# Kernel tuning notes

Measured on AMD Instinct MI355X. Metric: run time of the kernel, lower is better.

Reference implementation:

```python
import jax, jax.numpy as jnp
import numpy as np

B, S, D, H = 8, 1024, 768, 12
DH = D // H
EPS = 1e-5


def setup_inputs() -> dict:
    key = jax.random.key(0)
    ks = jax.random.split(key, 12)
    sc_h = 1.0 / np.sqrt(DH)
    sc_d = 1.0 / np.sqrt(D)
    return {
        "x": jax.random.normal(ks[0], (B, S, D), jnp.float32),
        "ln1_g": jnp.ones((D,), jnp.float32),
        "ln1_b": jnp.zeros((D,), jnp.float32),
        "Wq": jax.random.normal(ks[1], (H, DH, DH), jnp.float32) * sc_h,
        "bq": jax.random.normal(ks[2], (H, DH), jnp.float32) * 0.01,
        "Wk": jax.random.normal(ks[3], (H, DH, DH), jnp.float32) * sc_h,
        "bk": jax.random.normal(ks[4], (H, DH), jnp.float32) * 0.01,
        "Wv": jax.random.normal(ks[5], (H, DH, DH), jnp.float32) * sc_h,
        "bv": jax.random.normal(ks[6], (H, DH), jnp.float32) * 0.01,
        "ln2_g": jnp.ones((D,), jnp.float32),
        "ln2_b": jnp.zeros((D,), jnp.float32),
        "W1": jax.random.normal(ks[7], (D, 4 * D), jnp.float32) * sc_d,  # c_fc (bias=False)
        "W2": jax.random.normal(ks[8], (4 * D, D), jnp.float32) * (1.0 / np.sqrt(4 * D)),  # c_proj (bias=False)
    }


def _layernorm(x, g, b):
    m = jnp.mean(x, axis=-1, keepdims=True)
    v = jnp.mean(jnp.square(x - m), axis=-1, keepdims=True)
    return (x - m) * jax.lax.rsqrt(v + EPS) * g + b


def _msa(x, Wq, bq, Wk, bk, Wv, bv):
    b, s, d = x.shape
    h = x.reshape(b, s, H, DH)  # per-head slices of the embedding
    q = jnp.einsum('bshd,hde->bhse', h, Wq) + bq[None, :, None, :]
    k = jnp.einsum('bshd,hde->bhse', h, Wk) + bk[None, :, None, :]
    v = jnp.einsum('bshd,hde->bhse', h, Wv) + bv[None, :, None, :]
    scores = jnp.einsum('bhse,bhte->bhst', q, k) / np.sqrt(DH).astype(np.float32)
    attn = jax.nn.softmax(scores, axis=-1)
    o = jnp.einsum('bhst,bhte->bhse', attn, v)
    return o.transpose(0, 2, 1, 3).reshape(b, s, d)  # concat heads


def reference(x, ln1_g, ln1_b, Wq, bq, Wk, bk, Wv, bv, ln2_g, ln2_b, W1, W2):
    out = x + _msa(_layernorm(x, ln1_g, ln1_b), Wq, bq, Wk, bk, Wv, bv)
    h = _layernorm(out, ln2_g, ln2_b)
    ffn = jnp.dot(jax.nn.gelu(jnp.dot(h, W1), approximate=False), W2)
    return out + ffn
```

## Files before the change

kernel.cpp:

```cpp
#include <hip/hip_runtime.h>
#include <hip/hip_bf16.h>
#include <math.h>

#define B_ 8
#define S_ 1024
#define D_ 768
#define H_ 12
#define QSCALE 0.18033688011112042f

typedef __attribute__((ext_vector_type(8))) short short8;
typedef __attribute__((ext_vector_type(4))) float floatx4;
typedef unsigned short ushort_t;

__device__ __forceinline__ ushort_t f2bf(float f) {
  unsigned int u = __builtin_bit_cast(unsigned int, f);
  u += 0x7fffu + ((u >> 16) & 1u);
  return (ushort_t)(u >> 16);
}

__device__ __forceinline__ unsigned int pkbf(float a, float b) {
  __hip_bfloat162 h = __float22bfloat162_rn(make_float2(a, b));
  unsigned int r;
  __builtin_memcpy(&r, &h, sizeof(r));
  return r;
}

__global__ __launch_bounds__(256) void ln_bf16(
    const float* __restrict__ in, const float* __restrict__ g,
    const float* __restrict__ bias, ushort_t* __restrict__ out) {
  const int row = blockIdx.x * 4 + (threadIdx.x >> 6);
  const int lane = threadIdx.x & 63;
  const float* p = in + (size_t)row * D_;
  float4 v[3];
#pragma unroll
  for (int j = 0; j < 3; ++j) v[j] = *(const float4*)(p + j * 256 + lane * 4);
  float s = 0.f;
#pragma unroll
  for (int j = 0; j < 3; ++j) s += (v[j].x + v[j].y) + (v[j].z + v[j].w);
#pragma unroll
  for (int m = 1; m < 64; m <<= 1) s += __shfl_xor(s, m);
  const float mean = s * (1.0f / D_);
  float q = 0.f;
#pragma unroll
  for (int j = 0; j < 3; ++j) {
    const float a = v[j].x - mean, b = v[j].y - mean;
    const float c = v[j].z - mean, d = v[j].w - mean;
    q += (a * a + b * b) + (c * c + d * d);
  }
#pragma unroll
  for (int m = 1; m < 64; m <<= 1) q += __shfl_xor(q, m);
  const float rstd = rsqrtf(q * (1.0f / D_) + 1e-5f);
  ushort_t* o = out + (size_t)row * D_;
#pragma unroll
  for (int j = 0; j < 3; ++j) {
    const float4 gv = *(const float4*)(g + j * 256 + lane * 4);
    const float4 bv = *(const float4*)(bias + j * 256 + lane * 4);
    const unsigned int p01 = pkbf((v[j].x - mean) * rstd * gv.x + bv.x,
                                  (v[j].y - mean) * rstd * gv.y + bv.y);
    const unsigned int p23 = pkbf((v[j].z - mean) * rstd * gv.z + bv.z,
                                  (v[j].w - mean) * rstd * gv.w + bv.w);
    *(uint2*)(o + j * 256 + lane * 4) = make_uint2(p01, p23);
  }
}

__global__ __launch_bounds__(256) void transpose_cast(
    const float* __restrict__ W, ushort_t* __restrict__ Wt, int Kdim, int Ndim) {
  __shared__ float tile[32][33];
  const int n0 = blockIdx.x * 32, k0 = blockIdx.y * 32;
  const int tx = threadIdx.x & 31, ty = threadIdx.x >> 5;
#pragma unroll
  for (int i = 0; i < 32; i += 8)
    tile[ty + i][tx] = W[(size_t)(k0 + ty + i) * Ndim + n0 + tx];
  __syncthreads();
#pragma unroll
  for (int i = 0; i < 32; i += 8)
    Wt[(size_t)(n0 + ty + i) * Kdim + k0 + tx] = f2bf(tile[tx][ty + i]);
}

__global__ __launch_bounds__(256) void trans_w64(
    const float* __restrict__ Wq, const float* __restrict__ Wk,
    const float* __restrict__ Wv, ushort_t* __restrict__ Wqt,
    ushort_t* __restrict__ Wkt, ushort_t* __restrict__ Wvt) {
  const int h = blockIdx.x;
  const float* W = blockIdx.y == 0 ? Wq : blockIdx.y == 1 ? Wk : Wv;
  ushort_t* O = blockIdx.y == 0 ? Wqt : blockIdx.y == 1 ? Wkt : Wvt;
  __shared__ float t[64][65];
  const int tid = threadIdx.x;
#pragma unroll
  for (int i = 0; i < 16; ++i) {
    const int idx = tid + i * 256;
    t[idx >> 6][idx & 63] = W[h * 4096 + idx];
  }
  __syncthreads();
#pragma unroll
  for (int i = 0; i < 16; ++i) {
    const int idx = tid + i * 256;
    O[h * 4096 + idx] = f2bf(t[idx & 63][idx >> 6]);
  }
}

__global__ __launch_bounds__(256) void qkv_mfma(
    const ushort_t* __restrict__ xbf,
    const ushort_t* __restrict__ Wqt, const ushort_t* __restrict__ Wkt,
    const ushort_t* __restrict__ Wvt,
    const float* __restrict__ bq, const float* __restrict__ bk,
    const float* __restrict__ bv,
    ushort_t* __restrict__ qo, ushort_t* __restrict__ ko,
    ushort_t* __restrict__ vt) {
  const int h = blockIdx.y;
  const int mb = blockIdx.x * 128;
  const int tid = threadIdx.x;
  const int wave = tid >> 6, lane = tid & 63;
  const int lc = lane & 15, kq = lane >> 4;
  const int wm = wave * 32;

  short8 af[2][2];
#pragma unroll
  for (int mi = 0; mi < 2; ++mi)
#pragma unroll
    for (int kc = 0; kc < 2; ++kc)
      af[mi][kc] = *(const short8*)(xbf + (size_t)(mb + wm + mi * 16 + lc) * D_ +
                                    h * 64 + kc * 32 + kq * 8);

  const ushort_t* Wp[3] = {Wqt + h * 4096, Wkt + h * 4096, Wvt + h * 4096};
  floatx4 acc[3][2][4] = {};
#pragma unroll
  for (int w3 = 0; w3 < 3; ++w3)
#pragma unroll
    for (int n = 0; n < 4; ++n)
#pragma unroll
      for (int kc = 0; kc < 2; ++kc) {
        const short8 bfv =
            *(const short8*)(Wp[w3] + (n * 16 + lc) * 64 + kc * 32 + kq * 8);
#pragma unroll
        for (int mi = 0; mi < 2; ++mi)
          acc[w3][mi][n] = __builtin_amdgcn_mfma_f32_16x16x32_bf16(
              af[mi][kc], bfv, acc[w3][mi][n], 0, 0, 0);
      }

  const int b = mb >> 10;
  const size_t obase = (size_t)(b * H_ + h) * (S_ * 64);
#pragma unroll
  for (int w3 = 0; w3 < 2; ++w3) {
    const float* bias = (w3 == 0 ? bq : bk) + h * 64;
    ushort_t* outp = w3 == 0 ? qo : ko;
#pragma unroll
    for (int n = 0; n < 4; ++n) {
      const int e = n * 16 + lc;
      const float bvv = bias[e];
#pragma unroll
      for (int mi = 0; mi < 2; ++mi)
#pragma unroll
        for (int r = 0; r < 4; ++r) {
          const int sl = (mb & 1023) + wm + mi * 16 + kq * 4 + r;
          float v = acc[w3][mi][n][r] + bvv;
          if (w3 == 0) v *= QSCALE;
          outp[obase + (size_t)sl * 64 + e] = f2bf(v);
        }
    }
  }
#pragma unroll
  for (int n = 0; n < 4; ++n) {
    const int e = n * 16 + lc;
    const float bvv = bv[h * 64 + e];
#pragma unroll
    for (int mi = 0; mi < 2; ++mi) {
      const int sl0 = (mb & 1023) + wm + mi * 16 + kq * 4;
      const unsigned int p01 =
          pkbf(acc[2][mi][n][0] + bvv, acc[2][mi][n][1] + bvv);
      const unsigned int p23 =
          pkbf(acc[2][mi][n][2] + bvv, acc[2][mi][n][3] + bvv);
      *(uint2*)(vt + obase + (size_t)e * S_ + sl0) = make_uint2(p01, p23);
    }
  }
}

__global__ __launch_bounds__(256) void attn_mfma(
    const ushort_t* __restrict__ qb, const ushort_t* __restrict__ kb,
    const ushort_t* __restrict__ vt, const float* __restrict__ x,
    float* __restrict__ out1) {
  const int bh = blockIdx.x;
  const int tid = threadIdx.x;
  const int wave = tid >> 6, lane = tid & 63;
  const int lc = lane & 15, kq = lane >> 4;
  const int q0 = blockIdx.y * 128 + wave * 32;

  __shared__ __align__(16) ushort_t Ks[64 * 64];
  __shared__ __align__(16) ushort_t Vs[64 * 64];
  __shared__ __align__(16) ushort_t Pw[4][2][16 * 72];

  const ushort_t* qp = qb + (size_t)bh * (S_ * 64);
  const ushort_t* kp = kb + (size_t)bh * (S_ * 64);
  const ushort_t* vp = vt + (size_t)bh * (S_ * 64);

  short8 qf[2][2];
#pragma unroll
  for (int qi = 0; qi < 2; ++qi)
#pragma unroll
    for (int kc = 0; kc < 2; ++kc)
      qf[qi][kc] = *(const short8*)(qp + (size_t)(q0 + qi * 16 + lc) * 64 +
                                    kc * 32 + kq * 8);

  const int srow = tid >> 3;
  const int sgc = ((tid & 7) ^ (srow & 7)) * 8;
  const int slds = srow * 64 + (tid & 7) * 8;
  const int swz = lc & 7;

  float l_r[2] = {0.0f, 0.0f};
  floatx4 oacc[2][4] = {};

  for (int kt = 0; kt < 16; ++kt) {
#pragma unroll
    for (int half = 0; half < 2; ++half) {
      const int r = half * 32 + srow;
      __builtin_amdgcn_global_load_lds(
          (const __attribute__((address_space(1))) unsigned int*)
              (kp + (size_t)(kt * 64 + r) * 64 + sgc),
          (__attribute__((address_space(3))) unsigned int*)
              (Ks + half * 2048 + slds), 16, 0, 0);
      __builtin_amdgcn_global_load_lds(
          (const __attribute__((address_space(1))) unsigned int*)
              (vp + (size_t)r * S_ + kt * 64 + sgc),
          (__attribute__((address_space(3))) unsigned int*)
              (Vs + half * 2048 + slds), 16, 0, 0);
    }
    __syncthreads();

    floatx4 sacc[2][4] = {};
#pragma unroll
    for (int mi = 0; mi < 4; ++mi) {
      const int row = (mi * 16 + lc) * 64;
#pragma unroll
      for (int kc = 0; kc < 2; ++kc) {
        const short8 kf =
            *(const short8*)(Ks + row + ((kc * 4 + kq) ^ swz) * 8);
        sacc[0][mi] = __builtin_amdgcn_mfma_f32_16x16x32_bf16(
            kf, qf[0][kc], sacc[0][mi], 0, 0, 0);
        sacc[1][mi] = __builtin_amdgcn_mfma_f32_16x16x32_bf16(
            kf, qf[1][kc], sacc[1][mi], 0, 0, 0);
      }
    }

#pragma unroll
    for (int qi = 0; qi < 2; ++qi) {
      float pr[4][4];
      float sm = 0.f;
#pragma unroll
      for (int mi = 0; mi < 4; ++mi)
#pragma unroll
        for (int r = 0; r < 4; ++r) {
          pr[mi][r] = exp2f(sacc[qi][mi][r]);
          sm += pr[mi][r];
        }
      l_r[qi] += sm;
#pragma unroll
      for (int mi = 0; mi < 4; ++mi) {
        const unsigned int p01 = pkbf(pr[mi][0], pr[mi][1]);
        const unsigned int p23 = pkbf(pr[mi][2], pr[mi][3]);
        *(uint2*)(&Pw[wave][qi][lc * 72 + mi * 16 + kq * 4]) =
            make_uint2(p01, p23);
      }
    }
    asm volatile("s_waitcnt lgkmcnt(0)" ::: "memory");

    short8 pf[2][2];
#pragma unroll
    for (int qi = 0; qi < 2; ++qi)
#pragma unroll
      for (int kc = 0; kc < 2; ++kc)
        pf[qi][kc] =
            *(const short8*)(&Pw[wave][qi][lc * 72 + kc * 32 + kq * 8]);
#pragma unroll
    for (int mi = 0; mi < 4; ++mi) {
      const int row = (mi * 16 + lc) * 64;
#pragma unroll
      for (int kc = 0; kc < 2; ++kc) {
        const short8 vf =
            *(const short8*)(Vs + row + ((kc * 4 + kq) ^ swz) * 8);
        oacc[0][mi] = __builtin_amdgcn_mfma_f32_16x16x32_bf16(
            vf, pf[0][kc], oacc[0][mi], 0, 0, 0);
        oacc[1][mi] = __builtin_amdgcn_mfma_f32_16x16x32_bf16(
            vf, pf[1][kc], oacc[1][mi], 0, 0, 0);
      }
    }
    __syncthreads();
  }

  const int b = bh / H_, h = bh % H_;
  float* Ow = (float*)&Pw[wave][0][0];
#pragma unroll
  for (int qi = 0; qi < 2; ++qi) {
    float lt = l_r[qi];
    lt += __shfl_xor(lt, 16);
    lt += __shfl_xor(lt, 32);
    const float inv = 1.0f / lt;
#pragma unroll
    for (int mi = 0; mi < 4; ++mi) {
      floatx4 ov = oacc[qi][mi];
      ov[0] *= inv; ov[1] *= inv; ov[2] *= inv; ov[3] *= inv;
      *(floatx4*)(&Ow[lc * 68 + mi * 16 + kq * 4]) = ov;
    }
    asm volatile("s_waitcnt lgkmcnt(0)" ::: "memory");
    const int row = (lane >> 3) & 7, c8 = (lane & 7) * 4;
#pragma unroll
    for (int rg = 0; rg < 2; ++rg) {
      const int qq = rg * 8 + row;
      const size_t gbase =
          ((size_t)(b * S_) + q0 + qi * 16 + qq) * D_ + h * 64 + c8;
#pragma unroll
      for (int j = 0; j < 2; ++j) {
        const float4 ov = *(const float4*)(&Ow[qq * 68 + j * 32 + c8]);
        const float4 xv = *(const float4*)(x + gbase + j * 32);
        *(float4*)(out1 + gbase + j * 32) =
            make_float4(ov.x + xv.x, ov.y + xv.y, ov.z + xv.z, ov.w + xv.w);
      }
    }
    asm volatile("s_waitcnt lgkmcnt(0)" ::: "memory");
  }
}

template <int N, int K, bool GELU, bool RESID, bool OUT_BF16>
__global__ __launch_bounds__(256) void mfma_gemm(
    const ushort_t* __restrict__ A, const ushort_t* __restrict__ Bt,
    const float* __restrict__ resid, void* __restrict__ Cout) {
  const int mb = blockIdx.y * 128;
  const int nb = blockIdx.x * 128;
  const int tid = threadIdx.x;
  const int wave = tid >> 6, lane = tid & 63;
  const int wm = (wave >> 1) * 64, wn = (wave & 1) * 64;

  __shared__ ushort_t Asp[128 * 32];
  __shared__ ushort_t Bsp[128 * 32];

  const int srow = wave * 16 + (lane >> 2);
  const int skoff = (lane & 3) * 8;

  floatx4 acc[4][4] = {};

  for (int kb = 0; kb < K; kb += 32) {
#pragma unroll
    for (int j = 0; j < 2; ++j) {
      const int row = j * 64 + srow;
      __builtin_amdgcn_global_load_lds(
          (const __attribute__((address_space(1))) unsigned int*)
              (A + (size_t)(mb + row) * K + kb + skoff),
          (__attribute__((address_space(3))) unsigned int*)
              (Asp + (size_t)row * 32 + skoff),
          16, 0, 0);
      __builtin_amdgcn_global_load_lds(
          (const __attribute__((address_space(1))) unsigned int*)
              (Bt + (size_t)(nb + row) * K + kb + skoff),
          (__attribute__((address_space(3))) unsigned int*)
              (Bsp + (size_t)row * 32 + skoff),
          16, 0, 0);
    }
    __syncthreads();

    const short8* As8 = (const short8*)Asp;
    const short8* Bs8 = (const short8*)Bsp;
    const int lrow = lane & 15, lkq = lane >> 4;
    short8 af[4], bfr[4];
#pragma unroll
    for (int i = 0; i < 4; ++i) {
      af[i]  = As8[(wm + i * 16 + lrow) * 4 + lkq];
      bfr[i] = Bs8[(wn + i * 16 + lrow) * 4 + lkq];
    }
#pragma unroll
    for (int i = 0; i < 4; ++i)
#pragma unroll
      for (int j = 0; j < 4; ++j)
        acc[i][j] = __builtin_amdgcn_mfma_f32_16x16x32_bf16(
            af[i], bfr[j], acc[i][j], 0, 0, 0);
    __syncthreads();
  }

  const int lcol = lane & 15, lr4 = (lane >> 4) * 4;
#pragma unroll
  for (int i = 0; i < 4; ++i)
#pragma unroll
    for (int r = 0; r < 4; ++r) {
      const int m = mb + wm + i * 16 + lr4 + r;
#pragma unroll
      for (int j = 0; j < 4; ++j) {
        const int col = nb + wn + j * 16 + lcol;
        float vv = acc[i][j][r];
        if (GELU) vv = 0.5f * vv * (1.0f + erff(vv * 0.70710678f));
        if (RESID) vv += resid[(size_t)m * N + col];
        if (OUT_BF16)
          ((ushort_t*)Cout)[(size_t)m * N + col] = f2bf(vv);
        else
          ((float*)Cout)[(size_t)m * N + col] = vv;
      }
    }
}

template <int N, int K>
__global__ __launch_bounds__(256) void mfma_gemm2(
    const ushort_t* __restrict__ A, const ushort_t* __restrict__ Bt,
    const float* __restrict__ resid, float* __restrict__ C) {
  const int lin = blockIdx.x;
  const int xcd = lin & 7, slot = lin >> 3;
  const int mbg = slot / 6, nbi = slot - mbg * 6;
  const int mb = (xcd * 16 + mbg) * 64;
  const int nb = nbi * 128;
  const int tid = threadIdx.x;
  const int wave = tid >> 6, lane = tid & 63;
  const int wm = (wave >> 1) * 32, wn = (wave & 1) * 64;

  __shared__ __align__(16) ushort_t Asp[64 * 64];
  __shared__ __align__(16) ushort_t Bsp[128 * 64];

  const int sr = tid >> 3;
  const int sc8 = (tid & 7) * 8;
  const int sgx = ((tid & 7) ^ (sr & 7)) * 8;

  floatx4 acc[2][4] = {};

  for (int kb = 0; kb < K; kb += 64) {
#pragma unroll
    for (int j = 0; j < 2; ++j) {
      const int row = j * 32 + sr;
      __builtin_amdgcn_global_load_lds(
          (const __attribute__((address_space(1))) unsigned int*)
              (A + (size_t)(mb + row) * K + kb + sgx),
          (__attribute__((address_space(3))) unsigned int*)
              (Asp + row * 64 + sc8), 16, 0, 0);
    }
#pragma unroll
    for (int j = 0; j < 4; ++j) {
      const int row = j * 32 + sr;
      __builtin_amdgcn_global_load_lds(
          (const __attribute__((address_space(1))) unsigned int*)
              (Bt + (size_t)(nb + row) * K + kb + sgx),
          (__attribute__((address_space(3))) unsigned int*)
              (Bsp + row * 64 + sc8), 16, 0, 0);
    }
    __syncthreads();

    const int lc = lane & 15, kq = lane >> 4, swz = lc & 7;
    short8 af[2][2], bfr[4][2];
#pragma unroll
    for (int i = 0; i < 2; ++i)
#pragma unroll
      for (int ks = 0; ks < 2; ++ks)
        af[i][ks] = *(const short8*)(Asp + (wm + i * 16 + lc) * 64 +
                                     ((ks * 4 + kq) ^ swz) * 8);
#pragma unroll
    for (int j = 0; j < 4; ++j)
#pragma unroll
      for (int ks = 0; ks < 2; ++ks)
        bfr[j][ks] = *(const short8*)(Bsp + (wn + j * 16 + lc) * 64 +
                                      ((ks * 4 + kq) ^ swz) * 8);
#pragma unroll
    for (int ks = 0; ks < 2; ++ks)
#pragma unroll
      for (int i = 0; i < 2; ++i)
#pragma unroll
        for (int j = 0; j < 4; ++j)
          acc[i][j] = __builtin_amdgcn_mfma_f32_16x16x32_bf16(
              af[i][ks], bfr[j][ks], acc[i][j], 0, 0, 0);
    __syncthreads();
  }

  const int lcol = lane & 15, lr4 = (lane >> 4) * 4;
#pragma unroll
  for (int i = 0; i < 2; ++i)
#pragma unroll
    for (int r = 0; r < 4; ++r) {
      const int m = mb + wm + i * 16 + lr4 + r;
#pragma unroll
      for (int j = 0; j < 4; ++j) {
        const int col = nb + wn + j * 16 + lcol;
        C[(size_t)m * N + col] =
            acc[i][j][r] + resid[(size_t)m * N + col];
      }
    }
}

extern "C" void kernel_launch(void* const* d_in, const int* in_sizes, int n_in,
                              void* d_out, int out_size, void* d_ws, size_t ws_size,
                              hipStream_t stream) {
  (void)in_sizes; (void)n_in; (void)out_size; (void)ws_size;
  const float* x     = (const float*)d_in[0];
  const float* ln1_g = (const float*)d_in[1];
  const float* ln1_b = (const float*)d_in[2];
  const float* Wq    = (const float*)d_in[3];
  const float* bq    = (const float*)d_in[4];
  const float* Wk    = (const float*)d_in[5];
  const float* bk    = (const float*)d_in[6];
  const float* Wv    = (const float*)d_in[7];
  const float* bv    = (const float*)d_in[8];
  const float* ln2_g = (const float*)d_in[9];
  const float* ln2_b = (const float*)d_in[10];
  const float* W1    = (const float*)d_in[11];
  const float* W2    = (const float*)d_in[12];
  float* out = (float*)d_out;

  const size_t n = (size_t)B_ * S_ * D_;
  ushort_t* u = (ushort_t*)d_ws;
  ushort_t* xbf  = u;
  ushort_t* qb   = xbf + n;
  ushort_t* kb   = qb + n;
  ushort_t* vt   = kb + n;
  ushort_t* xbf2 = vt + n;
  ushort_t* act  = xbf2 + n;
  ushort_t* Wt1  = act + (size_t)8192 * 3072;
  ushort_t* Wt2  = Wt1 + (size_t)3072 * 768;
  ushort_t* Wqt  = Wt2 + (size_t)768 * 3072;
  ushort_t* Wkt  = Wqt + H_ * 4096;
  ushort_t* Wvt  = Wkt + H_ * 4096;
  float* out1 = (float*)(Wvt + H_ * 4096);

  trans_w64<<<dim3(12, 3), dim3(256), 0, stream>>>(Wq, Wk, Wv, Wqt, Wkt, Wvt);
  transpose_cast<<<dim3(96, 24), dim3(256), 0, stream>>>(W1, Wt1, 768, 3072);
  transpose_cast<<<dim3(24, 96), dim3(256), 0, stream>>>(W2, Wt2, 3072, 768);
  ln_bf16<<<dim3(2048), dim3(256), 0, stream>>>(x, ln1_g, ln1_b, xbf);
  qkv_mfma<<<dim3(64, 12), dim3(256), 0, stream>>>(xbf, Wqt, Wkt, Wvt,
                                                   bq, bk, bv, qb, kb, vt);
  attn_mfma<<<dim3(96, 8), dim3(256), 0, stream>>>(qb, kb, vt, x, out1);
  ln_bf16<<<dim3(2048), dim3(256), 0, stream>>>(out1, ln2_g, ln2_b, xbf2);
  mfma_gemm<3072, 768, true, false, true>
      <<<dim3(24, 64), dim3(256), 0, stream>>>(xbf2, Wt1, nullptr, act);
  mfma_gemm2<768, 3072>
      <<<dim3(768), dim3(256), 0, stream>>>(act, Wt2, out1, out);
}
```

Baseline: 306.2 us.

## Unify FFN GEMMs into double-buffered pipelined kernel with fast GELU

```diff
diff --git a/kernel.cpp b/kernel.cpp
--- a/kernel.cpp
+++ b/kernel.cpp
@@ -23,6 +23,28 @@
   unsigned int r;
   __builtin_memcpy(&r, &h, sizeof(r));
   return r;
+}
+
+__device__ __forceinline__ float gelu_f(float x) {
+  const float z = fabsf(x) * 0.70710678118654752f;
+  const float t = __builtin_amdgcn_rcpf(1.0f + 0.3275911f * z);
+  const float p =
+      t * (0.254829592f +
+           t * (-0.284496736f +
+                t * (1.421413741f + t * (-1.453152027f + t * 1.061405429f))));
+  const float e = __expf(-z * z);
+  const float erfv = 1.0f - p * e;
+  return 0.5f * x * (1.0f + copysignf(erfv, x));
+}
+
+template <int N>
+__device__ __forceinline__ void wait_vmcnt() {
+  if constexpr (N == 0)
+    asm volatile("s_waitcnt vmcnt(0)" ::: "memory");
+  else if constexpr (N == 6)
+    asm volatile("s_waitcnt vmcnt(6)" ::: "memory");
+  else
+    asm volatile("s_waitcnt vmcnt(8)" ::: "memory");
 }
 
 __global__ __launch_bounds__(256) void ln_bf16(
@@ -319,160 +341,128 @@
   }
 }
 
-template <int N, int K, bool GELU, bool RESID, bool OUT_BF16>
-__global__ __launch_bounds__(256) void mfma_gemm(
+template <int BM, int BN, int N, int K, bool GELU, bool RESID, bool OUT_BF16,
+          bool XCDMAP>
+__global__ __launch_bounds__(256) void gemm_pipe(
     const ushort_t* __restrict__ A, const ushort_t* __restrict__ Bt,
     const float* __restrict__ resid, void* __restrict__ Cout) {
-  const int mb = blockIdx.y * 128;
-  const int nb = blockIdx.x * 128;
+  constexpr int MI = BM / 32;
+  constexpr int NJ = BN / 32;
+  constexpr int LPT = (BM + BN) / 32;
+  constexpr int NT = K / 64;
+
+  int mb, nb;
+  if constexpr (XCDMAP) {
+    const int lin = blockIdx.x;
+    const int xcd = lin & 7, slot = lin >> 3;
+    const int mbg = slot / (N / 128), nbi = slot - mbg * (N / 128);
+    mb = (xcd * 16 + mbg) * 64;
+    nb = nbi * 128;
+  } else {
+    nb = blockIdx.x * BN;
+    mb = blockIdx.y * BM;
+  }
+
   const int tid = threadIdx.x;
   const int wave = tid >> 6, lane = tid & 63;
-  const int wm = (wave >> 1) * 64, wn = (wave & 1) * 64;
-
-  __shared__ ushort_t Asp[128 * 32];
-  __shared__ ushort_t Bsp[128 * 32];
-
-  const int srow = wave * 16 + (lane >> 2);
-  const int skoff = (lane & 3) * 8;
-
-  floatx4 acc[4][4] = {};
-
-  for (int kb = 0; kb < K; kb += 32) {
-#pragma unroll
-    for (int j = 0; j < 2; ++j) {
-      const int row = j * 64 + srow;
+  const int wm = (wave >> 1) * (BM / 2), wn = (wave & 1) * (BN / 2);
+
+  __shared__ __align__(16) ushort_t Asp[2][BM * 64];
+  __shared__ __align__(16) ushort_t Bsp[2][BN * 64];
+
+  const int sr = tid >> 3;
+  const int sc8 = (tid & 7) * 8;
+  const int sgx = ((tid & 7) ^ (sr & 7)) * 8;
+
+  auto stage = [&](int t, int buf) {
+    const int kb = t * 64;
+#pragma unroll
+    for (int j = 0; j < BM / 32; ++j) {
+      const int row = j * 32 + sr;
       __builtin_amdgcn_global_load_lds(
           (const __attribute__((address_space(1))) unsigned int*)
-              (A + (size_t)(mb + row) * K + kb + skoff),
+              (A + (size_t)(mb + row) * K + kb + sgx),
           (__attribute__((address_space(3))) unsigned int*)
-              (Asp + (size_t)row * 32 + skoff),
-          16, 0, 0);
+              (&Asp[buf][row * 64 + sc8]), 16, 0, 0);
+    }
+#pragma unroll
+    for (int j = 0; j < BN / 32; ++j) {
+      const int row = j * 32 + sr;
       __builtin_amdgcn_global_load_lds(
           (const __attribute__((address_space(1))) unsigned int*)
-              (Bt + (size_t)(nb + row) * K + kb + skoff),
+              (Bt + (size_t)(nb + row) * K + kb + sgx),
           (__attribute__((address_space(3))) unsigned int*)
-              (Bsp + (size_t)row * 32 + skoff),
-          16, 0, 0);
-    }
-    __syncthreads();
-
-    const short8* As8 = (const short8*)Asp;
-    const short8* Bs8 = (const short8*)Bsp;
-    const int lrow = lane & 15, lkq = lane >> 4;
-    short8 af[4], bfr[4];
-#pragma unroll
-    for (int i = 0; i < 4; ++i) {
-      af[i]  = As8[(wm + i * 16 + lrow) * 4 + lkq];
-      bfr[i] = Bs8[(wn + i * 16 + lrow) * 4 + lkq];
-    }
-#pragma unroll
-    for (int i = 0; i < 4; ++i)
-#pragma unroll
-      for (int j = 0; j < 4; ++j)
-        acc[i][j] = __builtin_amdgcn_mfma_f32_16x16x32_bf16(
-            af[i], bfr[j], acc[i][j], 0, 0, 0);
-    __syncthreads();
+              (&Bsp[buf][row * 64 + sc8]), 16, 0, 0);
+    }
+  };
+
+  stage(0, 0);
+  stage(1, 1);
+  wait_vmcnt<LPT>();
+  __builtin_amdgcn_s_barrier();
+  __builtin_amdgcn_sched_barrier(0);
+
+  const int lc = lane & 15, kq = lane >> 4, swz = lc & 7;
+  floatx4 acc[MI][NJ] = {};
+
+#pragma unroll 1
+  for (int t = 0; t < NT; ++t) {
+    const int cur = t & 1;
+    short8 af[MI][2], bfr[NJ][2];
+#pragma unroll
+    for (int i = 0; i < MI; ++i)
+#pragma unroll
+      for (int ks = 0; ks < 2; ++ks)
+        af[i][ks] = *(const short8*)(&Asp[cur][(wm + i * 16 + lc) * 64 +
+                                               ((ks * 4 + kq) ^ swz) * 8]);
+#pragma unroll
+    for (int j = 0; j < NJ; ++j)
+#pragma unroll
+      for (int ks = 0; ks < 2; ++ks)
+        bfr[j][ks] = *(const short8*)(&Bsp[cur][(wn + j * 16 + lc) * 64 +
+                                                ((ks * 4 + kq) ^ swz) * 8]);
+    asm volatile("s_waitcnt lgkmcnt(0)" ::: "memory");
+    __builtin_amdgcn_sched_barrier(0);
+    __builtin_amdgcn_s_barrier();
+    __builtin_amdgcn_sched_barrier(0);
+    if (t + 2 < NT) stage(t + 2, cur);
+    __builtin_amdgcn_sched_barrier(0);
+    __builtin_amdgcn_s_setprio(1);
+#pragma unroll
+    for (int ks = 0; ks < 2; ++ks)
+#pragma unroll
+      for (int i = 0; i < MI; ++i)
+#pragma unroll
+        for (int j = 0; j < NJ; ++j)
+          acc[i][j] = __builtin_amdgcn_mfma_f32_16x16x32_bf16(
+              af[i][ks], bfr[j][ks], acc[i][j], 0, 0, 0);
+    __builtin_amdgcn_s_setprio(0);
+    if (t + 2 < NT)
+      wait_vmcnt<LPT>();
+    else if (t + 1 < NT)
+      wait_vmcnt<0>();
+    if (t + 1 < NT) {
+      __builtin_amdgcn_s_barrier();
+      __builtin_amdgcn_sched_barrier(0);
+    }
   }
 
   const int lcol = lane & 15, lr4 = (lane >> 4) * 4;
 #pragma unroll
-  for (int i = 0; i < 4; ++i)
+  for (int i = 0; i < MI; ++i)
 #pragma unroll
     for (int r = 0; r < 4; ++r) {
       const int m = mb + wm + i * 16 + lr4 + r;
 #pragma unroll
-      for (int j = 0; j < 4; ++j) {
+      for (int j = 0; j < NJ; ++j) {
         const int col = nb + wn + j * 16 + lcol;
         float vv = acc[i][j][r];
-        if (GELU) vv = 0.5f * vv * (1.0f + erff(vv * 0.70710678f));
+        if (GELU) vv = gelu_f(vv);
         if (RESID) vv += resid[(size_t)m * N + col];
         if (OUT_BF16)
           ((ushort_t*)Cout)[(size_t)m * N + col] = f2bf(vv);
         else
           ((float*)Cout)[(size_t)m * N + col] = vv;
-      }
-    }
-}
-
-template <int N, int K>
-__global__ __launch_bounds__(256) void mfma_gemm2(
-    const ushort_t* __restrict__ A, const ushort_t* __restrict__ Bt,
-    const float* __restrict__ resid, float* __restrict__ C) {
-  const int lin = blockIdx.x;
-  const int xcd = lin & 7, slot = lin >> 3;
-  const int mbg = slot / 6, nbi = slot - mbg * 6;
-  const int mb = (xcd * 16 + mbg) * 64;
-  const int nb = nbi * 128;
-  const int tid = threadIdx.x;
-  const int wave = tid >> 6, lane = tid & 63;
-  const int wm = (wave >> 1) * 32, wn = (wave & 1) * 64;
-
-  __shared__ __align__(16) ushort_t Asp[64 * 64];
-  __shared__ __align__(16) ushort_t Bsp[128 * 64];
-
-  const int sr = tid >> 3;
-  const int sc8 = (tid & 7) * 8;
-  const int sgx = ((tid & 7) ^ (sr & 7)) * 8;
-
-  floatx4 acc[2][4] = {};
-
-  for (int kb = 0; kb < K; kb += 64) {
-#pragma unroll
-    for (int j = 0; j < 2; ++j) {
-      const int row = j * 32 + sr;
-      __builtin_amdgcn_global_load_lds(
-          (const __attribute__((address_space(1))) unsigned int*)
-              (A + (size_t)(mb + row) * K + kb + sgx),
-          (__attribute__((address_space(3))) unsigned int*)
-              (Asp + row * 64 + sc8), 16, 0, 0);
-    }
-#pragma unroll
-    for (int j = 0; j < 4; ++j) {
-      const int row = j * 32 + sr;
-      __builtin_amdgcn_global_load_lds(
-          (const __attribute__((address_space(1))) unsigned int*)
-              (Bt + (size_t)(nb + row) * K + kb + sgx),
-          (__attribute__((address_space(3))) unsigned int*)
-              (Bsp + row * 64 + sc8), 16, 0, 0);
-    }
-    __syncthreads();
-
-    const int lc = lane & 15, kq = lane >> 4, swz = lc & 7;
-    short8 af[2][2], bfr[4][2];
-#pragma unroll
-    for (int i = 0; i < 2; ++i)
-#pragma unroll
-      for (int ks = 0; ks < 2; ++ks)
-        af[i][ks] = *(const short8*)(Asp + (wm + i * 16 + lc) * 64 +
-                                     ((ks * 4 + kq) ^ swz) * 8);
-#pragma unroll
-    for (int j = 0; j < 4; ++j)
-#pragma unroll
-      for (int ks = 0; ks < 2; ++ks)
-        bfr[j][ks] = *(const short8*)(Bsp + (wn + j * 16 + lc) * 64 +
-                                      ((ks * 4 + kq) ^ swz) * 8);
-#pragma unroll
-    for (int ks = 0; ks < 2; ++ks)
-#pragma unroll
-      for (int i = 0; i < 2; ++i)
-#pragma unroll
-        for (int j = 0; j < 4; ++j)
-          acc[i][j] = __builtin_amdgcn_mfma_f32_16x16x32_bf16(
-              af[i][ks], bfr[j][ks], acc[i][j], 0, 0, 0);
-    __syncthreads();
-  }
-
-  const int lcol = lane & 15, lr4 = (lane >> 4) * 4;
-#pragma unroll
-  for (int i = 0; i < 2; ++i)
-#pragma unroll
-    for (int r = 0; r < 4; ++r) {
-      const int m = mb + wm + i * 16 + lr4 + r;
-#pragma unroll
-      for (int j = 0; j < 4; ++j) {
-        const int col = nb + wn + j * 16 + lcol;
-        C[(size_t)m * N + col] =
-            acc[i][j][r] + resid[(size_t)m * N + col];
       }
     }
 }
@@ -519,8 +509,8 @@
                                                    bq, bk, bv, qb, kb, vt);
   attn_mfma<<<dim3(96, 8), dim3(256), 0, stream>>>(qb, kb, vt, x, out1);
   ln_bf16<<<dim3(2048), dim3(256), 0, stream>>>(out1, ln2_g, ln2_b, xbf2);
-  mfma_gemm<3072, 768, true, false, true>
+  gemm_pipe<128, 128, 3072, 768, true, false, true, false>
       <<<dim3(24, 64), dim3(256), 0, stream>>>(xbf2, Wt1, nullptr, act);
-  mfma_gemm2<768, 3072>
+  gemm_pipe<64, 128, 768, 3072, false, true, false, true>
       <<<dim3(768), dim3(256), 0, stream>>>(act, Wt2, out1, out);
 }
```

New measurement: 292.9 us. 4.3% less time.
